# Kernel optimization log

Measured on AMD Instinct MI355X. Metric: run time of the kernel, lower is better.

## Reference

```python
import jax, jax.numpy as jnp
import numpy as np

A = 9          # angRes
MIND = -4      # mindisp
MAXD = 4       # maxdisp
C0 = A // 2
BDR = C0 * MAXD  # per-view zero padding


def setup_inputs() -> dict:
    key = jax.random.key(0)
    k1, k2, k3 = jax.random.split(key, 3)
    b, c, h, w = 1, 32, 192, 192
    cout = 128
    x = jax.random.normal(k1, (b, c, A * A, h, w), dtype=jnp.float32)
    mask = jax.random.uniform(k2, (b, A * A, h, w), dtype=jnp.float32)
    W = jax.random.normal(k3, (cout, A * A), dtype=jnp.float32) / np.sqrt(A * A)
    return {"x": x, "mask": mask, "W": W}


def reference(x, mask, W):
    # x: [b, c, A*A, h, w], mask: [b, A*A, h, w], W: [cout, A*A] (grouped 1x1 conv, groups=c)
    b, c, aa, h, w = x.shape
    m = W.shape[0] // c  # outputs per group
    Wr = W.reshape(c, m, A, A)
    # per-view layout [b, a1, a2, c, h, w], zero-pad spatially by BDR (equivalent to mosaic padding)
    xv = x.reshape(b, c, A, A, h, w).transpose(0, 2, 3, 1, 4, 5)
    xp = jnp.pad(xv, ((0, 0), (0, 0), (0, 0), (0, 0), (BDR, BDR), (BDR, BDR)))
    maskv = mask.reshape(b, A, A, h, w)
    mask_avg = jnp.mean(mask, axis=1)  # [b, h, w]
    ar = jnp.arange(A)
    outs = []
    for d in range(MIND, MAXD + 1):
        # tap (p,q) of the dilated AxA unfold reads padded view (p,q) shifted by start_p/start_q
        starts = C0 * (d - MIND) - ar * d                      # [A]
        ridx = starts[:, None] + jnp.arange(h)[None, :]        # [A, h]
        cidx = starts[:, None] + jnp.arange(w)[None, :]        # [A, w]
        t = jnp.take_along_axis(xp, ridx[None, :, None, None, :, None], axis=4)
        t = jnp.take_along_axis(t, cidx[None, None, :, None, None, :], axis=5)  # [b,A,A,c,h,w]
        # fuse mask modulation + grouped 1x1 conv over the A*A taps
        o = jnp.einsum('bpqchw,bpqhw,cmpq->bcmhw', t, maskv, Wr)
        outs.append(o.reshape(b, c * m, h, w) / mask_avg[:, None, :, :])
    return jnp.stack(outs, axis=2)  # [b, cout, n_disp, h, w]
```

## Files before the change

### kernel.cpp

```cpp
#include <hip/hip_runtime.h>


#define AA   81
#define HH   192
#define WW   192
#define HW   (HH * WW)
#define NC   32
#define MM   4
#define ND   9

__global__ __launch_bounds__(256)
void buildcost_kernel(const float* __restrict__ x,
                      const float* __restrict__ mask,
                      const float* __restrict__ Wt,
                      float* __restrict__ out) {
    __shared__ float wlds[AA * MM];

    const int c  = blockIdx.z;
    const int tx = threadIdx.x & 15;
    const int ty = threadIdx.x >> 4;
    const int j  = blockIdx.x * 16 + tx;
    const int i  = blockIdx.y * 16 + ty;
    const int pix = i * WW + j;

    for (int idx = threadIdx.x; idx < AA * MM; idx += 256) {
        const int t = idx >> 2;
        const int m = idx & 3;
        wlds[idx] = Wt[(c * MM + m) * AA + t];
    }
    __syncthreads();

    const float* __restrict__ xc = x + (size_t)c * AA * HW;

    float acc[ND][MM];
#pragma unroll
    for (int dd = 0; dd < ND; ++dd)
#pragma unroll
        for (int m = 0; m < MM; ++m) acc[dd][m] = 0.f;

    float msum = 0.f;

    int p = 0, q = 0;
#pragma unroll 1
    for (int t = 0; t < AA; ++t) {
        const float mval = mask[t * HW + pix];
        msum += mval;
        const float4 w4 = *(const float4*)&wlds[t * 4];
        const int kp = 4 - p;
        const int kq = 4 - q;
        const float* __restrict__ xt = xc + t * HW;

#pragma unroll
        for (int dd = 0; dd < ND; ++dd) {
            const int d  = dd - 4;
            const int y  = i + kp * d;
            const int xx = j + kq * d;
            float v = 0.f;
            if ((unsigned)y < (unsigned)HH && (unsigned)xx < (unsigned)WW)
                v = xt[y * WW + xx];
            const float s = v * mval;
            acc[dd][0] += s * w4.x;
            acc[dd][1] += s * w4.y;
            acc[dd][2] += s * w4.z;
            acc[dd][3] += s * w4.w;
        }

        if (++q == 9) { q = 0; ++p; }
    }

    const float inv = (float)AA / msum;

#pragma unroll
    for (int m = 0; m < MM; ++m)
#pragma unroll
        for (int dd = 0; dd < ND; ++dd)
            out[((size_t)(c * MM + m) * ND + dd) * HW + pix] = acc[dd][m] * inv;
}

extern "C" void kernel_launch(void* const* d_in, const int* in_sizes, int n_in,
                              void* d_out, int out_size, void* d_ws, size_t ws_size,
                              hipStream_t stream) {
    const float* x    = (const float*)d_in[0];
    const float* mask = (const float*)d_in[1];
    const float* Wt   = (const float*)d_in[2];
    float* out        = (float*)d_out;

    dim3 grid(WW / 16, HH / 16, NC);
    dim3 block(256);
    buildcost_kernel<<<grid, block, 0, stream>>>(x, mask, Wt, out);
}
```

Baseline: 878.5 us.

## Remap blocks so each channel stays on one XCD; add unchecked interior path

The 3D grid becomes a 1D grid. Block indices are decoded so that all spatial tiles of a given channel land on the same XCD, assuming round-robin dispatch across 8 XCDs. Neighbouring tiles then share that XCD's L2 for their overlapping shifted reads of the channel's 81 views. Interior tiles, where the largest disparity shift (16 px) cannot leave the image, also get a fast path that drops the per-tap bounds checks and uses a single strided base pointer. The cost is duplicated code and a dependence on the hardware's block-to-XCD dispatch order.

Result: no change. 876.7 us (-0.2%).

```diff
diff --git a/kernel.cpp b/kernel.cpp
--- a/kernel.cpp
+++ b/kernel.cpp
@@ -9,6 +9,7 @@
 #define MM   4
 #define ND   9
 
+
 __global__ __launch_bounds__(256)
 void buildcost_kernel(const float* __restrict__ x,
                       const float* __restrict__ mask,
@@ -16,11 +17,19 @@
                       float* __restrict__ out) {
     __shared__ float wlds[AA * MM];
 
-    const int c  = blockIdx.z;
+    const int lin  = blockIdx.x;
+    const int xcd  = lin & 7;
+    const int slot = lin >> 3;
+    const int cgrp = slot / 144;
+    const int sp   = slot - cgrp * 144;
+    const int c    = xcd + (cgrp << 3);
+    const int by   = sp / 12;
+    const int bx   = sp - by * 12;
+
     const int tx = threadIdx.x & 15;
     const int ty = threadIdx.x >> 4;
-    const int j  = blockIdx.x * 16 + tx;
-    const int i  = blockIdx.y * 16 + ty;
+    const int j  = bx * 16 + tx;
+    const int i  = by * 16 + ty;
     const int pix = i * WW + j;
 
     for (int idx = threadIdx.x; idx < AA * MM; idx += 256) {
@@ -40,32 +49,56 @@
 
     float msum = 0.f;
 
-    int p = 0, q = 0;
+    const bool interior = (bx >= 1) & (bx <= 10) & (by >= 1) & (by <= 10);
+
+    if (interior) {
+        int p = 0, q = 0;
 #pragma unroll 1
-    for (int t = 0; t < AA; ++t) {
-        const float mval = mask[t * HW + pix];
-        msum += mval;
-        const float4 w4 = *(const float4*)&wlds[t * 4];
-        const int kp = 4 - p;
-        const int kq = 4 - q;
-        const float* __restrict__ xt = xc + t * HW;
-
+        for (int t = 0; t < AA; ++t) {
+            const float mval = mask[t * HW + pix];
+            msum += mval;
+            const float4 w4 = *(const float4*)&wlds[t * 4];
+            const int kp = 4 - p;
+            const int kq = 4 - q;
+            const int step = kp * WW + kq;
+            const float* __restrict__ base = xc + (size_t)t * HW + pix;
 #pragma unroll
-        for (int dd = 0; dd < ND; ++dd) {
-            const int d  = dd - 4;
-            const int y  = i + kp * d;
-            const int xx = j + kq * d;
-            float v = 0.f;
-            if ((unsigned)y < (unsigned)HH && (unsigned)xx < (unsigned)WW)
-                v = xt[y * WW + xx];
-            const float s = v * mval;
-            acc[dd][0] += s * w4.x;
-            acc[dd][1] += s * w4.y;
-            acc[dd][2] += s * w4.z;
-            acc[dd][3] += s * w4.w;
+            for (int dd = 0; dd < ND; ++dd) {
+                const float v = base[(dd - 4) * step];
+                const float s = v * mval;
+                acc[dd][0] += s * w4.x;
+                acc[dd][1] += s * w4.y;
+                acc[dd][2] += s * w4.z;
+                acc[dd][3] += s * w4.w;
+            }
+            if (++q == 9) { q = 0; ++p; }
         }
-
-        if (++q == 9) { q = 0; ++p; }
+    } else {
+        int p = 0, q = 0;
+#pragma unroll 1
+        for (int t = 0; t < AA; ++t) {
+            const float mval = mask[t * HW + pix];
+            msum += mval;
+            const float4 w4 = *(const float4*)&wlds[t * 4];
+            const int kp = 4 - p;
+            const int kq = 4 - q;
+            const float* __restrict__ xt = xc + (size_t)t * HW;
+#pragma unroll
+            for (int dd = 0; dd < ND; ++dd) {
+                const int d  = dd - 4;
+                const int y  = i + kp * d;
+                const int xx = j + kq * d;
+                float v = 0.f;
+                if ((unsigned)y < (unsigned)HH && (unsigned)xx < (unsigned)WW)
+                    v = xt[y * WW + xx];
+                const float s = v * mval;
+                acc[dd][0] += s * w4.x;
+                acc[dd][1] += s * w4.y;
+                acc[dd][2] += s * w4.z;
+                acc[dd][3] += s * w4.w;
+            }
+            if (++q == 9) { q = 0; ++p; }
+        }
     }
 
     const float inv = (float)AA / msum;
@@ -85,7 +118,7 @@
     const float* Wt   = (const float*)d_in[2];
     float* out        = (float*)d_out;
 
-    dim3 grid(WW / 16, HH / 16, NC);
+    dim3 grid(12 * 12 * NC);
     dim3 block(256);
     buildcost_kernel<<<grid, block, 0, stream>>>(x, mask, Wt, out);
 }
```
